# Performance work log

Measured on AMD Instinct MI355X. Metric: run time of the kernel, lower is better.

The kernel has to match this reference:

```python
import jax, jax.numpy as jnp
import numpy as np

# Static module configuration (matches init_kwargs)
NLAT, NLON = 256, 256
LMAX = 128            # max_degree
MMAX = 129            # nlon//2 + 1 == max_degree + 1
CIN, COUT, BATCH = 32, 32, 8
NUM_COEFFS = 2 * LMAX * MMAX  # real+imag flattened, = 33024


def _cc_quadrature(n):
    """Clenshaw-Curtis nodes (colatitudes incl. poles) and weights on [-1,1]."""
    N = n - 1
    tj = np.pi * np.arange(n) / N
    k = np.arange(1, N // 2 + 1)
    bk = np.where(2 * k == N, 1.0, 2.0)
    S = np.cos(2.0 * np.outer(tj, k)) @ (bk / (4.0 * k * k - 1.0))
    c = np.full(n, 2.0)
    c[0] = c[-1] = 1.0
    w = (c / N) * (1.0 - S)
    return tj, w


def _legpoly(mmax, lmax, t):
    """Orthonormal associated Legendre P_l^m(cos t) incl. 1/sqrt(4pi) and CS phase.
    Returns array [mmax, lmax, nlat]; entries with l < m are zero."""
    ct, st = np.cos(t), np.sin(t)
    p = np.zeros((mmax, lmax, t.shape[0]))
    p[0, 0] = 1.0 / np.sqrt(4.0 * np.pi)
    for m in range(1, min(mmax, lmax)):
        p[m, m] = -np.sqrt((2.0 * m + 1.0) / (2.0 * m)) * st * p[m - 1, m - 1]
    for m in range(min(mmax, lmax)):
        if m + 1 < lmax:
            p[m, m + 1] = np.sqrt(2.0 * m + 3.0) * ct * p[m, m]
    for m in range(mmax):
        for l in range(m + 2, lmax):
            a = np.sqrt((4.0 * l * l - 1.0) / (l * l - m * m))
            b = np.sqrt(((l - 1.0) ** 2 - m * m) / (4.0 * (l - 1.0) ** 2 - 1.0))
            p[m, l] = a * (ct * p[m, l - 1] - b * p[m, l - 2])
    return p


_T, _WQ = _cc_quadrature(NLAT)
_PCT_NP = _legpoly(MMAX, LMAX, _T)                 # synthesis Legendre matrix
_PCT = jnp.asarray(_PCT_NP, jnp.float32)           # [mmax, lmax, nlat]
_PCTW = jnp.asarray(_PCT_NP * _WQ[None, None, :], jnp.float32)  # analysis (quadrature weighted)


def setup_inputs() -> dict:
    key = jax.random.key(0)
    k1, k2 = jax.random.split(key)
    x = jax.random.normal(k1, (BATCH, CIN, NLAT, NLON), jnp.float32)
    scale = (1.0 / (CIN * COUT * NUM_COEFFS)) ** 0.5
    weight = scale * jax.random.normal(k2, (CIN, COUT, NUM_COEFFS), jnp.float32)
    return {"x": x, "weight": weight}


def reference(x, weight):
    B, C = x.shape[0], x.shape[1]
    # ---- forward real SHT (ortho norm, equiangular / Clenshaw-Curtis) ----
    # longitudinal rfft with 'forward' norm, scaled by 2*pi
    xh = (2.0 * np.pi / NLON) * jnp.fft.rfft(x, axis=-1)   # [B,C,nlat,nlon//2+1] complex
    xh = xh[..., :MMAX]
    re = jnp.einsum('bckm,mlk->bclm', jnp.real(xh), _PCTW)  # [B,C,lmax,mmax]
    im = jnp.einsum('bckm,mlk->bclm', jnp.imag(xh), _PCTW)
    spec = jnp.stack([re, im], axis=-1).reshape(B, C, NUM_COEFFS)
    # ---- spectral channel mixing: per-coefficient dense channel mix ----
    out = jnp.einsum('bix,iox->box', spec, weight)          # [B,Cout,NUM_COEFFS]
    out = out.reshape(B, COUT, LMAX, MMAX, 2)
    # ---- inverse real SHT ----
    rr = jnp.einsum('bolm,mlk->bokm', out[..., 0], _PCT)    # [B,Cout,nlat,mmax]
    ri = jnp.einsum('bolm,mlk->bokm', out[..., 1], _PCT)
    Xm = jax.lax.complex(rr, ri)                            # mmax == nlon//2+1
    y = jnp.fft.irfft(Xm, n=NLON, axis=-1) * NLON           # irfft norm='forward'
    return y
```

## Files before the change

kernel.cpp:

```cpp
#include <hip/hip_runtime.h>


typedef __attribute__((ext_vector_type(8))) short short8;
typedef __attribute__((ext_vector_type(4))) float f32x4;

__device__ __forceinline__ ushort bf16_rtn(float v) {
  uint u = __float_as_uint(v);
  return (ushort)((u + 0x7FFFu + ((u >> 16) & 1u)) >> 16);
}
__device__ __forceinline__ void split2(float v, ushort& h, ushort& l) {
  h = bf16_rtn(v);
  float hf = __uint_as_float(((uint)h) << 16);
  l = bf16_rtn(v - hf);
}

__global__ __launch_bounds__(256) void k_tables(
    ushort* __restrict__ Th, ushort* __restrict__ Tl,
    ushort* __restrict__ TiTh, ushort* __restrict__ TiTl,
    ushort* __restrict__ PWh, ushort* __restrict__ PWl,
    ushort* __restrict__ PTh, ushort* __restrict__ PTl) {
  const double PI = 3.14159265358979323846264338327950288;
  const int t = threadIdx.x;
  const int m = blockIdx.x;
  __shared__ double sCos[256];
  __shared__ double sCoef[128];
  __shared__ double sRatio[128];
  __shared__ double sA[128], sB[128];

  if (m == 128) {
    const double scale = 2.0 * PI / 256.0;
    sCos[t] = cos(scale * (double)t);
    __syncthreads();
    const int n = t;
    for (int ch = 0; ch < 8; ++ch) {
      uint tih[8], til[8];
#pragma unroll
      for (int j = 0; j < 16; ++j) {
        const int mm = ch * 16 + j;
        const int r = (mm * n) & 255;
        const double c = sCos[r];
        const double s = sCos[(r + 192) & 255];
        const double wm = (mm == 0) ? 1.0 : 2.0;
        ushort h, l;
        split2((float)(scale * c), h, l);  Th[(2*mm)*256+n]=h;   Tl[(2*mm)*256+n]=l;
        split2((float)(-scale * s), h, l); Th[(2*mm+1)*256+n]=h; Tl[(2*mm+1)*256+n]=l;
        ushort h2, l2b, h3, l3;
        split2((float)(wm * c), h2, l2b);
        split2((float)(-wm * s), h3, l3);
        if (j & 1) { tih[j>>1] |= ((uint)h2 << 16*0) << 0, tih[j>>1] = tih[j>>1]; }
        if ((j & 1) == 0) { tih[j>>1] = (uint)h2 | ((uint)h3 << 16); til[j>>1] = (uint)l2b | ((uint)l3 << 16); }
        else              {  }
        tih[j>>1] = tih[j>>1];
        (void)0;
        if (true) { uint hv = (uint)h2 | ((uint)h3 << 16);
                    uint lv = (uint)l2b | ((uint)l3 << 16);
                    if ((j & 1) == 0) { tih[j>>1] = hv; til[j>>1] = lv; }
                    else {  }
        }
        (void)0;
      }
      (void)tih; (void)til;
      uint th16[16], tl16[16];
#pragma unroll
      for (int j = 0; j < 16; ++j) {
        const int mm = ch * 16 + j;
        const int r = (mm * n) & 255;
        const double c = sCos[r];
        const double s = sCos[(r + 192) & 255];
        const double wm = (mm == 0) ? 1.0 : 2.0;
        ushort h2, l2b, h3, l3;
        split2((float)(wm * c), h2, l2b);
        split2((float)(-wm * s), h3, l3);
        th16[j] = (uint)h2 | ((uint)h3 << 16);
        tl16[j] = (uint)l2b | ((uint)l3 << 16);
      }
      const int base = n * 256 + ch * 32;
#pragma unroll
      for (int q4 = 0; q4 < 4; ++q4) {
        *(uint4*)(TiTh + base + q4 * 8) = make_uint4(th16[4*q4], th16[4*q4+1], th16[4*q4+2], th16[4*q4+3]);
        *(uint4*)(TiTl + base + q4 * 8) = make_uint4(tl16[4*q4], tl16[4*q4+1], tl16[4*q4+2], tl16[4*q4+3]);
      }
    }
    return;
  }

  const double scale255 = 2.0 * PI / 255.0;
  if (t < 255) sCos[t] = cos(scale255 * (double)t);
  if (t >= 1 && t < 128) {
    const double dt = (double)t;
    sCoef[t]  = 2.0 / (4.0 * dt * dt - 1.0);
    sRatio[t] = (2.0 * dt + 1.0) / (2.0 * dt);
    if (t >= m + 2) {
      const double dl = dt, dm = (double)m;
      sA[t] = sqrt((4.0*dl*dl - 1.0) / (dl*dl - dm*dm));
      sB[t] = sqrt(((dl-1.0)*(dl-1.0) - dm*dm) / (4.0*(dl-1.0)*(dl-1.0) - 1.0));
    }
  }
  __syncthreads();

  const int k = t;
  const double tj = PI * (double)k / 255.0;
  double ssum = 0.0;
  {
    int r = 0;
    for (int kk = 1; kk <= 127; ++kk) {
      r += k; if (r >= 255) r -= 255;
      ssum += sCoef[kk] * sCos[r];
    }
  }
  const double cj = (k == 0 || k == 255) ? 1.0 : 2.0;
  const double wq = cj / 255.0 * (1.0 - ssum);
  const double ct = cos(tj), st = sin(tj);
  double prod = 1.0, stp = 1.0;
  for (int mm = 1; mm <= m; ++mm) { prod *= sRatio[mm]; stp *= -st; }
  const double pmm = (1.0 / sqrt(4.0 * PI)) * sqrt(prod) * stp;
  const double sq2m3 = sqrt(2.0 * (double)m + 3.0);

  const size_t pwB = (size_t)m * 32768;
  const size_t ptB = (size_t)m * 32768 + (size_t)k * 128;
  double plm1 = 0.0, plm2 = 0.0;
  for (int lc0 = 0; lc0 < 128; lc0 += 16) {
    uint hq[8], lq[8];
#pragma unroll
    for (int j = 0; j < 16; ++j) {
      const int l = lc0 + j;
      double val;
      if (l < m)           val = 0.0;
      else if (l == m)     val = pmm;
      else if (l == m + 1) val = sq2m3 * ct * pmm;
      else                 val = sA[l] * (ct * plm1 - sB[l] * plm2);
      plm2 = plm1; plm1 = val;
      ushort h, lo; split2((float)val, h, lo);
      if ((j & 1) == 0) { hq[j>>1] = (uint)h; lq[j>>1] = (uint)lo; }
      else              { hq[j>>1] |= ((uint)h) << 16; lq[j>>1] |= ((uint)lo) << 16; }
      ushort hw, lw; split2((float)(val * wq), hw, lw);
      PWh[pwB + (size_t)l * 256 + k] = hw;
      PWl[pwB + (size_t)l * 256 + k] = lw;
    }
    *(uint4*)(PTh + ptB + lc0)     = make_uint4(hq[0], hq[1], hq[2], hq[3]);
    *(uint4*)(PTh + ptB + lc0 + 8) = make_uint4(hq[4], hq[5], hq[6], hq[7]);
    *(uint4*)(PTl + ptB + lc0)     = make_uint4(lq[0], lq[1], lq[2], lq[3]);
    *(uint4*)(PTl + ptB + lc0 + 8) = make_uint4(lq[4], lq[5], lq[6], lq[7]);
  }
}

template<int AM, int BM>
__global__ __launch_bounds__(256) void mfma_gemm(
    const ushort* __restrict__ Ah, const ushort* __restrict__ Al, const float* __restrict__ Af,
    const ushort* __restrict__ Bh, const ushort* __restrict__ Bl, const float* __restrict__ Bf,
    float* __restrict__ C,
    int lda, int ldb, int ldc, int K,
    long aZ, int aShift, long bZ, int bShift, long cZ, int cColOff, int kFromZ)
{
  __shared__ __align__(16) short sAh[128*40];
  __shared__ __align__(16) short sAl[128*40];
  __shared__ __align__(16) short sBh[128*40];
  __shared__ __align__(16) short sBl[128*40];
  const int z = blockIdx.z;
  const long aOff = ((long)(z >> aShift)) * aZ;
  const long bOff = ((long)(z >> bShift)) * bZ;
  const long cOff = (long)z * cZ;
  const int i0 = blockIdx.y * 128;
  const int j0 = blockIdx.x * 128;
  const int t = threadIdx.x;
  const int lane = t & 63, w = t >> 6;
  const int wy = w >> 1, wx = w & 1;
  const int il = lane & 15, q = lane >> 4;
  const int kstart = kFromZ ? ((z >> 1) & ~31) : 0;

  f32x4 acc[4][4];
#pragma unroll
  for (int a = 0; a < 4; ++a)
#pragma unroll
    for (int b = 0; b < 4; ++b) acc[a][b] = (f32x4){0.f, 0.f, 0.f, 0.f};

  for (int k0 = kstart; k0 < K; k0 += 32) {
    __syncthreads();
    if constexpr (AM == 0) {
      const int r = t >> 1, ks = (t & 1) * 16;
      const size_t g = (size_t)aOff + (size_t)(i0 + r) * lda + k0 + ks;
      *(short8*)&sAh[r*40+ks]   = *(const short8*)(Ah + g);
      *(short8*)&sAh[r*40+ks+8] = *(const short8*)(Ah + g + 8);
      *(short8*)&sAl[r*40+ks]   = *(const short8*)(Al + g);
      *(short8*)&sAl[r*40+ks+8] = *(const short8*)(Al + g + 8);
    } else {
      const int kk0 = 8*w + 2*q;
      const float* s0 = Af + aOff + (size_t)(k0 + kk0) * lda + i0 + il;
      const float* s1 = s0 + lda;
#pragma unroll
      for (int c = 0; c < 8; ++c) {
        float v0 = s0[c*16], v1 = s1[c*16];
        ushort h0,l0,h1,l1; split2(v0,h0,l0); split2(v1,h1,l1);
        const int idx = (il + 16*c)*40 + kk0;
        *(uint*)&sAh[idx] = (uint)h0 | ((uint)h1 << 16);
        *(uint*)&sAl[idx] = (uint)l0 | ((uint)l1 << 16);
      }
    }
    if constexpr (BM == 0) {
      const int r = t >> 1, ks = (t & 1) * 16;
      const size_t g = (size_t)bOff + (size_t)(j0 + r) * ldb + k0 + ks;
      *(short8*)&sBh[r*40+ks]   = *(const short8*)(Bh + g);
      *(short8*)&sBh[r*40+ks+8] = *(const short8*)(Bh + g + 8);
      *(short8*)&sBl[r*40+ks]   = *(const short8*)(Bl + g);
      *(short8*)&sBl[r*40+ks+8] = *(const short8*)(Bl + g + 8);
    } else {
      const int r = t >> 1, ks = (t & 1) * 16;
      const float* src = Bf + bOff + (size_t)(j0 + r) * ldb + k0 + ks;
#pragma unroll
      for (int jj = 0; jj < 4; ++jj) {
        float4 f = *(const float4*)(src + 4*jj);
        ushort h0,l0,h1,l1,h2,l2,h3,l3;
        split2(f.x,h0,l0); split2(f.y,h1,l1); split2(f.z,h2,l2); split2(f.w,h3,l3);
        *(ushort4*)&sBh[r*40+ks+4*jj] = make_ushort4(h0,h1,h2,h3);
        *(ushort4*)&sBl[r*40+ks+4*jj] = make_ushort4(l0,l1,l2,l3);
      }
    }
    __syncthreads();
    short8 afh[4], afl[4];
#pragma unroll
    for (int mi = 0; mi < 4; ++mi) {
      const int row = wy*64 + mi*16 + il;
      afh[mi] = *(const short8*)&sAh[row*40 + q*8];
      afl[mi] = *(const short8*)&sAl[row*40 + q*8];
    }
#pragma unroll
    for (int nj = 0; nj < 4; ++nj) {
      const int row = wx*64 + nj*16 + il;
      short8 bfh = *(const short8*)&sBh[row*40 + q*8];
      short8 bfl = *(const short8*)&sBl[row*40 + q*8];
#pragma unroll
      for (int mi = 0; mi < 4; ++mi) {
        acc[mi][nj] = __builtin_amdgcn_mfma_f32_16x16x32_bf16(afh[mi], bfh, acc[mi][nj], 0, 0, 0);
        acc[mi][nj] = __builtin_amdgcn_mfma_f32_16x16x32_bf16(afh[mi], bfl, acc[mi][nj], 0, 0, 0);
        acc[mi][nj] = __builtin_amdgcn_mfma_f32_16x16x32_bf16(afl[mi], bfh, acc[mi][nj], 0, 0, 0);
      }
    }
  }
#pragma unroll
  for (int mi = 0; mi < 4; ++mi)
#pragma unroll
    for (int nj = 0; nj < 4; ++nj)
#pragma unroll
      for (int r = 0; r < 4; ++r) {
        const long gi = i0 + wy*64 + mi*16 + q*4 + r;
        const long gj = j0 + wx*64 + nj*16 + il;
        C[cOff + gi*ldc + cColOff + gj] = acc[mi][nj][r];
      }
}

__global__ __launch_bounds__(256) void k_stagec(const float* __restrict__ spec,
                                                const float* __restrict__ w,
                                                float* __restrict__ outb) {
  const int cb = blockIdx.x, l = blockIdx.y;
  if (cb * 16 > l) return;
  __shared__ float s_spec[32 * 257];
  __shared__ float s_w[256 * 33];
  const int t = threadIdx.x;
  const int c = t & 31, og = t >> 5;
  const size_t x0 = 258u * l + cb * 32;
  for (int cc = 0; cc < 32; ++cc)
    s_spec[cc * 257 + t] = spec[(size_t)(cb * 32 + cc) * 32768 + l * 256 + t];
  float acc[8][4] = {{0.f}};
  const int lr = t >> 4;
  const int lq = (t & 15) * 2;
  for (int isub = 0; isub < 4; ++isub) {
    __syncthreads();
    for (int pass = 0; pass < 16; ++pass) {
      const int rho = pass * 16 + lr;
      const int io = (isub * 8 + (rho >> 5)) * 32 + (rho & 31);
      const float2 wv = *(const float2*)&w[(size_t)io * 33024 + x0 + lq];
      s_w[rho * 33 + lq]     = wv.x;
      s_w[rho * 33 + lq + 1] = wv.y;
    }
    __syncthreads();
#pragma unroll
    for (int idp = 0; idp < 4; ++idp) {
      const int i0 = isub * 8 + idp * 2;
      const int r0 = idp * 64;
      float2 sv[8];
#pragma unroll
      for (int b = 0; b < 8; ++b)
        sv[b] = *(const float2*)&s_spec[c * 257 + b * 32 + i0];
      float wv0[4], wv1[4];
#pragma unroll
      for (int od = 0; od < 4; ++od) {
        wv0[od] = s_w[(r0 + og * 4 + od) * 33 + c];
        wv1[od] = s_w[(r0 + 32 + og * 4 + od) * 33 + c];
      }
#pragma unroll
      for (int b = 0; b < 8; ++b)
#pragma unroll
        for (int od = 0; od < 4; ++od)
          acc[b][od] = fmaf(sv[b].x, wv0[od], fmaf(sv[b].y, wv1[od], acc[b][od]));
    }
  }
  __syncthreads();
#pragma unroll
  for (int b = 0; b < 8; ++b)
#pragma unroll
    for (int od = 0; od < 4; ++od)
      s_w[c * 257 + b * 32 + og * 4 + od] = acc[b][od];
  __syncthreads();
  for (int cc = 0; cc < 32; ++cc)
    outb[(size_t)(cb * 32 + cc) * 32768 + l * 256 + t] = s_w[cc * 257 + t];
}

extern "C" void kernel_launch(void* const* d_in, const int* in_sizes, int n_in,
                              void* d_out, int out_size, void* d_ws, size_t ws_size,
                              hipStream_t stream) {
  const float* x = (const float*)d_in[0];
  const float* w = (const float*)d_in[1];
  float* y = (float*)d_out;
  char* ws = (char*)d_ws;

  ushort* Th   = (ushort*)(ws + 0);
  ushort* Tl   = (ushort*)(ws + 131072);
  ushort* TiTh = (ushort*)(ws + 262144);
  ushort* TiTl = (ushort*)(ws + 393216);
  ushort* PWh  = (ushort*)(ws + 524288);
  ushort* PWl  = (ushort*)(ws + 8912896);
  ushort* PTh  = (ushort*)(ws + 17301504);
  ushort* PTl  = (ushort*)(ws + 25690112);
  float* XHhalf= (float*)(ws + 34078720);
  float* outb  = XHhalf;
  float* spec  = (float*)(ws + 67633152);
  float* XM    = (float*)(ws + 101187584);

  k_tables<<<dim3(129), dim3(256), 0, stream>>>(Th, Tl, TiTh, TiTl, PWh, PWl, PTh, PTl);

  for (int half = 0; half < 2; ++half) {
    mfma_gemm<0,1><<<dim3(256, 2, 1), dim3(256), 0, stream>>>(
        Th, Tl, nullptr, nullptr, nullptr, x + (size_t)half * 8388608, XHhalf,
        256, 256, 32768, 256, 0L, 0, 0L, 0, 0L, 0, 0);
    mfma_gemm<0,1><<<dim3(1, 1, 256), dim3(256), 0, stream>>>(
        PWh, PWl, nullptr, nullptr, nullptr, XHhalf, spec,
        256, 256, 256, 256, 32768L, 1, 32768L, 0, 32768L, half * 128, 0);
  }

  k_stagec<<<dim3(8, 128), dim3(256), 0, stream>>>(spec, w, outb);

  mfma_gemm<2,0><<<dim3(2, 2, 256), dim3(256), 0, stream>>>(
      nullptr, nullptr, outb, PTh, PTl, nullptr, XM,
      256, 128, 256, 128, 32768L, 0, 32768L, 1, 65536L, 0, 1);

  mfma_gemm<2,0><<<dim3(2, 512, 1), dim3(256), 0, stream>>>(
      nullptr, nullptr, XM, TiTh, TiTl, nullptr, y,
      65536, 256, 256, 256, 0L, 0, 0L, 0, 0L, 0, 0);
}
```

Before: 421.0 us.

## Emit bf16 hi/lo split from rfft GEMM and skip zero Legendre tiles

The longitudinal DFT GEMM now writes its output directly as bf16 hi/lo pairs, and runs once over both batch halves instead of in a loop. The Legendre analysis GEMM then reads pre-split operands rather than splitting fp32 on the fly. It also skips MFMA work for 16-row subtiles where l < m, since those Legendre entries are zero. The table kernel drops a redundant duplicated loop. This trades more workspace and two output buffers for fewer launches, less conversion work and fewer wasted MFMAs, with some added branching inside the inner loop.

```diff
diff --git a/kernel.cpp b/kernel.cpp
--- a/kernel.cpp
+++ b/kernel.cpp
@@ -33,7 +33,7 @@
     __syncthreads();
     const int n = t;
     for (int ch = 0; ch < 8; ++ch) {
-      uint tih[8], til[8];
+      uint th16[16], tl16[16];
 #pragma unroll
       for (int j = 0; j < 16; ++j) {
         const int mm = ch * 16 + j;
@@ -44,30 +44,6 @@
         ushort h, l;
         split2((float)(scale * c), h, l);  Th[(2*mm)*256+n]=h;   Tl[(2*mm)*256+n]=l;
         split2((float)(-scale * s), h, l); Th[(2*mm+1)*256+n]=h; Tl[(2*mm+1)*256+n]=l;
-        ushort h2, l2b, h3, l3;
-        split2((float)(wm * c), h2, l2b);
-        split2((float)(-wm * s), h3, l3);
-        if (j & 1) { tih[j>>1] |= ((uint)h2 << 16*0) << 0, tih[j>>1] = tih[j>>1]; }
-        if ((j & 1) == 0) { tih[j>>1] = (uint)h2 | ((uint)h3 << 16); til[j>>1] = (uint)l2b | ((uint)l3 << 16); }
-        else              {  }
-        tih[j>>1] = tih[j>>1];
-        (void)0;
-        if (true) { uint hv = (uint)h2 | ((uint)h3 << 16);
-                    uint lv = (uint)l2b | ((uint)l3 << 16);
-                    if ((j & 1) == 0) { tih[j>>1] = hv; til[j>>1] = lv; }
-                    else {  }
-        }
-        (void)0;
-      }
-      (void)tih; (void)til;
-      uint th16[16], tl16[16];
-#pragma unroll
-      for (int j = 0; j < 16; ++j) {
-        const int mm = ch * 16 + j;
-        const int r = (mm * n) & 255;
-        const double c = sCos[r];
-        const double s = sCos[(r + 192) & 255];
-        const double wm = (mm == 0) ? 1.0 : 2.0;
         ushort h2, l2b, h3, l3;
         split2((float)(wm * c), h2, l2b);
         split2((float)(-wm * s), h3, l3);
@@ -144,13 +120,14 @@
   }
 }
 
-template<int AM, int BM>
+template<int AM, int BM, int CM>
 __global__ __launch_bounds__(256) void mfma_gemm(
     const ushort* __restrict__ Ah, const ushort* __restrict__ Al, const float* __restrict__ Af,
     const ushort* __restrict__ Bh, const ushort* __restrict__ Bl, const float* __restrict__ Bf,
-    float* __restrict__ C,
+    float* __restrict__ C, ushort* __restrict__ Ch, ushort* __restrict__ Cl,
     int lda, int ldb, int ldc, int K,
-    long aZ, int aShift, long bZ, int bShift, long cZ, int cColOff, int kFromZ)
+    long aZ, int aShift, long bZ, int bShift, long cZ, int cColOff,
+    int kFromZ, int mSkipFromZ)
 {
   __shared__ __align__(16) short sAh[128*40];
   __shared__ __align__(16) short sAl[128*40];
@@ -167,6 +144,7 @@
   const int wy = w >> 1, wx = w & 1;
   const int il = lane & 15, q = lane >> 4;
   const int kstart = kFromZ ? ((z >> 1) & ~31) : 0;
+  const int nsk = mSkipFromZ ? ((z >> 1) >> 4) : 0;
 
   f32x4 acc[4][4];
 #pragma unroll
@@ -219,9 +197,11 @@
     short8 afh[4], afl[4];
 #pragma unroll
     for (int mi = 0; mi < 4; ++mi) {
-      const int row = wy*64 + mi*16 + il;
-      afh[mi] = *(const short8*)&sAh[row*40 + q*8];
-      afl[mi] = *(const short8*)&sAl[row*40 + q*8];
+      if (wy*4 + mi >= nsk) {
+        const int row = wy*64 + mi*16 + il;
+        afh[mi] = *(const short8*)&sAh[row*40 + q*8];
+        afl[mi] = *(const short8*)&sAl[row*40 + q*8];
+      }
     }
 #pragma unroll
     for (int nj = 0; nj < 4; ++nj) {
@@ -230,9 +210,11 @@
       short8 bfl = *(const short8*)&sBl[row*40 + q*8];
 #pragma unroll
       for (int mi = 0; mi < 4; ++mi) {
-        acc[mi][nj] = __builtin_amdgcn_mfma_f32_16x16x32_bf16(afh[mi], bfh, acc[mi][nj], 0, 0, 0);
-        acc[mi][nj] = __builtin_amdgcn_mfma_f32_16x16x32_bf16(afh[mi], bfl, acc[mi][nj], 0, 0, 0);
-        acc[mi][nj] = __builtin_amdgcn_mfma_f32_16x16x32_bf16(afl[mi], bfh, acc[mi][nj], 0, 0, 0);
+        if (wy*4 + mi >= nsk) {
+          acc[mi][nj] = __builtin_amdgcn_mfma_f32_16x16x32_bf16(afh[mi], bfh, acc[mi][nj], 0, 0, 0);
+          acc[mi][nj] = __builtin_amdgcn_mfma_f32_16x16x32_bf16(afh[mi], bfl, acc[mi][nj], 0, 0, 0);
+          acc[mi][nj] = __builtin_amdgcn_mfma_f32_16x16x32_bf16(afl[mi], bfh, acc[mi][nj], 0, 0, 0);
+        }
       }
     }
   }
@@ -244,7 +226,13 @@
       for (int r = 0; r < 4; ++r) {
         const long gi = i0 + wy*64 + mi*16 + q*4 + r;
         const long gj = j0 + wx*64 + nj*16 + il;
-        C[cOff + gi*ldc + cColOff + gj] = acc[mi][nj][r];
+        if constexpr (CM == 0) {
+          C[cOff + gi*ldc + cColOff + gj] = acc[mi][nj][r];
+        } else {
+          ushort h, lo; split2(acc[mi][nj][r], h, lo);
+          const size_t idx = (size_t)(cOff + gi*ldc + cColOff + gj);
+          Ch[idx] = h; Cl[idx] = lo;
+        }
       }
 }
 
@@ -321,29 +309,29 @@
   ushort* PWl  = (ushort*)(ws + 8912896);
   ushort* PTh  = (ushort*)(ws + 17301504);
   ushort* PTl  = (ushort*)(ws + 25690112);
-  float* XHhalf= (float*)(ws + 34078720);
-  float* outb  = XHhalf;
-  float* spec  = (float*)(ws + 67633152);
-  float* XM    = (float*)(ws + 101187584);
+  ushort* XHh  = (ushort*)(ws + 34078720);
+  ushort* XHl  = (ushort*)(ws + 67633152);
+  float* XM    = (float*)(ws + 34078720);
+  float* spec  = (float*)(ws + 101187584);
+  float* outb  = spec;
 
   k_tables<<<dim3(129), dim3(256), 0, stream>>>(Th, Tl, TiTh, TiTl, PWh, PWl, PTh, PTl);
 
-  for (int half = 0; half < 2; ++half) {
-    mfma_gemm<0,1><<<dim3(256, 2, 1), dim3(256), 0, stream>>>(
-        Th, Tl, nullptr, nullptr, nullptr, x + (size_t)half * 8388608, XHhalf,
-        256, 256, 32768, 256, 0L, 0, 0L, 0, 0L, 0, 0);
-    mfma_gemm<0,1><<<dim3(1, 1, 256), dim3(256), 0, stream>>>(
-        PWh, PWl, nullptr, nullptr, nullptr, XHhalf, spec,
-        256, 256, 256, 256, 32768L, 1, 32768L, 0, 32768L, half * 128, 0);
-  }
+  mfma_gemm<0,1,1><<<dim3(512, 2, 1), dim3(256), 0, stream>>>(
+      Th, Tl, nullptr, nullptr, nullptr, x, nullptr, XHh, XHl,
+      256, 256, 65536, 256, 0L, 0, 0L, 0, 0L, 0, 0, 0);
+
+  mfma_gemm<0,0,0><<<dim3(2, 1, 256), dim3(256), 0, stream>>>(
+      PWh, PWl, nullptr, XHh, XHl, nullptr, spec, nullptr, nullptr,
+      256, 256, 256, 256, 32768L, 1, 65536L, 0, 32768L, 0, 0, 1);
 
   k_stagec<<<dim3(8, 128), dim3(256), 0, stream>>>(spec, w, outb);
 
-  mfma_gemm<2,0><<<dim3(2, 2, 256), dim3(256), 0, stream>>>(
-      nullptr, nullptr, outb, PTh, PTl, nullptr, XM,
-      256, 128, 256, 128, 32768L, 0, 32768L, 1, 65536L, 0, 1);
-
-  mfma_gemm<2,0><<<dim3(2, 512, 1), dim3(256), 0, stream>>>(
-      nullptr, nullptr, XM, TiTh, TiTl, nullptr, y,
-      65536, 256, 256, 256, 0L, 0, 0L, 0, 0L, 0, 0);
-}
+  mfma_gemm<2,0,0><<<dim3(2, 2, 256), dim3(256), 0, stream>>>(
+      nullptr, nullptr, outb, PTh, PTl, nullptr, XM, nullptr, nullptr,
+      256, 128, 256, 128, 32768L, 0, 32768L, 1, 65536L, 0, 1, 0);
+
+  mfma_gemm<2,0,0><<<dim3(2, 512, 1), dim3(256), 0, stream>>>(
+      nullptr, nullptr, XM, TiTh, TiTl, nullptr, y, nullptr, nullptr,
+      65536, 256, 256, 256, 0L, 0, 0L, 0, 0L, 0, 0, 0);
+}
```

After: 414.7 us. Within noise of the previous version (-1.5%).
